# Optimization experiments

Measured on AMD Instinct MI355X. Metric: run time of the kernel, lower is better.

Reference implementation:

```python
import jax, jax.numpy as jnp
import numpy as np

ALPHA = 2.0


def _sq_edt_1d(f):
    """1D squared Euclidean distance transform along the last axis.
    f: (..., n) with 0 at 'sites' and a large value elsewhere.
    g[..., i] = min_j f[..., j] + (i - j)^2  (exact, brute-force lower envelope).
    Uses a scan over output index i to keep memory at O(size(f)).
    """
    n = f.shape[-1]
    idx = jnp.arange(n, dtype=f.dtype)

    def step(_, i):
        return None, jnp.min(f + (i - idx) ** 2, axis=-1)

    _, g = jax.lax.scan(step, None, idx)  # (n, ...)
    return jnp.moveaxis(g, 0, -1)


def _edt(mask):
    """Exact Euclidean distance transform of a boolean mask (b,1,X,Y,Z):
    distance from each True voxel to the nearest False voxel (scipy edt semantics).
    Separable squared-distance transform applied along each spatial axis.
    """
    spatial = mask.shape[2:]
    BIG = jnp.float32(sum(s * s for s in spatial) + 1)  # > any achievable sq dist
    f = jnp.where(mask, BIG, jnp.float32(0.0))
    for ax in range(2, mask.ndim):  # channel axis has size 1 -> contributes 0
        f = jnp.moveaxis(_sq_edt_1d(jnp.moveaxis(f, ax, -1)), -1, ax)
    return jnp.sqrt(f)


def _distance_field(img):
    fg = img > 0.5
    # per-sample guard: field is zero if a sample has no foreground
    fg_any = jnp.any(fg, axis=tuple(range(1, img.ndim)))  # (b,)
    field = _edt(fg) + _edt(~fg)
    shape = (-1,) + (1,) * (img.ndim - 1)
    return jnp.where(fg_any.reshape(shape), field, jnp.float32(0.0))


def setup_inputs() -> dict:
    key = jax.random.key(0)
    k1, k2 = jax.random.split(key)
    pred = jax.random.uniform(k1, (2, 1, 128, 128, 128), dtype=jnp.float32)
    target = jax.random.uniform(k2, (2, 1, 128, 128, 128), dtype=jnp.float32)
    return {"pred": pred, "target": target}


def reference(pred, target):
    # distance fields are computed under no_grad in the original
    pred_dt = jax.lax.stop_gradient(_distance_field(pred))
    target_dt = jax.lax.stop_gradient(_distance_field(target))

    pred_error = (pred - target) ** 2
    distance = pred_dt ** ALPHA + target_dt ** ALPHA
    dt_field = pred_error * distance
    return jnp.mean(dt_field)
```

## Files before the change

### kernel.cpp

```cpp
#include <hip/hip_runtime.h>


constexpr int BIGI = 49153;
constexpr int NVOX = 4194304;
constexpr int STZ  = 129;
constexpr int STX  = 65;

__device__ __forceinline__ void envelope_win(const unsigned int* __restrict__ p,
                                             const int stride, const float i0f,
                                             const int qlo, const int qhi,
                                             float acc[16]) {
    unsigned int vc = p[qlo * stride];
    float jm2 = -4.0f * (float)qlo;
    for (int q = qlo; q <= qhi; ++q) {
        unsigned int vn = p[(q + 1) * stride];
        float h0 = (float)(vc & 0xffffu);
        float h1 = (float)(vc >> 16);
        float jb = jm2 - 2.0f;
        float c0 = fmaf(jm2, i0f, h0);
        float c1 = fmaf(jb,  i0f, h1);
#pragma unroll
        for (int k = 0; k < 16; ++k) {
            acc[k] = fminf(acc[k], fminf(c0, c1));
            c0 += jm2; c1 += jb;
        }
        jm2 -= 4.0f;
        vc = vn;
    }
}

__device__ __forceinline__ int window_of(const unsigned int* __restrict__ p,
                                         const int stride, const int i0) {
    int fmx = 0;
#pragma unroll
    for (int m = 0; m < 8; ++m) {
        unsigned int v = p[((i0 >> 1) + m) * stride];
        int y0 = i0 + 2 * m, y1 = y0 + 1;
        int f0 = (int)(v & 0xffffu) - y0 * y0;
        int f1 = (int)(v >> 16) - y1 * y1;
        fmx = max(fmx, max(f0, f1));
    }
#pragma unroll
    for (int off = 32; off; off >>= 1) fmx = max(fmx, __shfl_xor(fmx, off));
    int W = (int)sqrtf((float)fmx);
    W += (W * W < fmx);
    W += (W * W < fmx);
    return W;
}

__global__ __launch_bounds__(512) void zy_kernel(const float* __restrict__ pred,
                                                 const float* __restrict__ tgt,
                                                 unsigned short* __restrict__ ws) {
    __shared__ unsigned int hz[65 * STZ];
    __shared__ unsigned long long bm[256];
    const int t   = blockIdx.x;
    const int pol = t & 1;
    const int img = (t >> 1) & 1;
    const int s   = t >> 2;
    const int b   = s >> 7;
    const int x   = s & 127;
    const int sb  = (b * 128 + x) * 16384;
    const int tid = threadIdx.x;
    const float* im = img ? tgt : pred;

    float vreg[32];
#pragma unroll
    for (int k = 0; k < 32; ++k) vreg[k] = im[sb + tid + k * 512];

#pragma unroll
    for (int k = 0; k < 32; ++k) {
        bool fg = vreg[k] > 0.5f;
        bool site = pol ? fg : !fg;
        unsigned long long bal = __ballot(site);
        if ((tid & 63) == 0) bm[(tid + k * 512) >> 6] = bal;
    }
    __syncthreads();

    unsigned short* hu = (unsigned short*)hz;
    const int z = tid & 127;
#pragma unroll
    for (int k = 0; k < 32; ++k) {
        int y = (tid >> 7) + k * 4;
        unsigned long long m0 = bm[2 * y], m1 = bm[2 * y + 1];
        int d;
        if (z < 64) {
            unsigned long long lm = m0 << (63 - z);
            unsigned long long rm = m0 >> z;
            int dfwd = lm ? __builtin_clzll(lm) : 999;
            int db0  = rm ? __builtin_ctzll(rm) : 999;
            int db1  = (m1 ? __builtin_ctzll(m1) : 999) + (64 - z);
            d = min(dfwd, min(db0, db1));
        } else {
            int zz = z - 64;
            unsigned long long lm = m1 << (63 - zz);
            unsigned long long rm = m1 >> zz;
            int df1 = lm ? __builtin_clzll(lm) : 999;
            int df0 = (m0 ? __builtin_clzll(m0) : 999) + zz + 1;
            int dbw = rm ? __builtin_ctzll(rm) : 999;
            d = min(min(df1, df0), dbw);
        }
        int f = (d <= 127) ? d * d : BIGI;
        hu[((y >> 1) * STZ) * 2 + (y & 1) + 2 * z] = (unsigned short)(f + y * y);
    }
    __syncthreads();

    unsigned short* outv = ws + (size_t)(img * 2 + pol) * NVOX + sb;
    const int c = tid & 127;
    const int xsq = x * x;
#pragma clang loop unroll(disable)
    for (int r = 0; r < 2; ++r) {
        const int i0 = (tid >> 7) * 16 + r * 64;
        const float i0f = (float)i0;
        const int W = window_of(hz + c, STZ, i0);
        const int qlo = __builtin_amdgcn_readfirstlane(max(0, (i0 - W) >> 1));
        const int qhi = __builtin_amdgcn_readfirstlane(min(63, (i0 + 15 + W) >> 1));
        float acc[16];
#pragma unroll
        for (int k = 0; k < 16; ++k) acc[k] = 3.0e38f;
        envelope_win(hz + c, STZ, i0f, qlo, qhi, acc);
#pragma unroll
        for (int k = 0; k < 16; ++k) {
            float iif = i0f + (float)k;
            outv[(i0 + k) * 128 + c] =
                (unsigned short)((unsigned int)fmaf(iif, iif, acc[k]) + xsq);
        }
    }
}

__global__ __launch_bounds__(512) void xloss_kernel(const float* __restrict__ pred,
                                                    const float* __restrict__ tgt,
                                                    const unsigned short* __restrict__ ws,
                                                    float* __restrict__ out) {
    __shared__ unsigned int hx[129 * STX];
    __shared__ float red[8];
    const int t    = blockIdx.x;
    const int img  = t & 1;
    const int b    = (t >> 1) & 1;
    const int q0   = (t >> 2) * 64;
    const int base = b * 2097152 + q0;
    const int tid  = threadIdx.x;
    const int c    = tid & 63;
    const int i0   = (tid >> 6) * 16;
    const float i0f = (float)i0;
    const unsigned short* A16 = ws + (size_t)(img * 2) * NVOX;
    const unsigned int* A32 = (const unsigned int*)(A16 + base);
    const unsigned int* B32 = (const unsigned int*)(A16 + NVOX + base);

    float dv[16];
#pragma unroll
    for (int k = 0; k < 16; ++k) {
        int v = base + (i0 + k) * 16384 + c;
        dv[k] = pred[v] - tgt[v];
    }

#pragma unroll
    for (int k = 0; k < 8; ++k) {
        int l = tid + k * 512;
        int j = l >> 5, cp = l & 31;
        unsigned int va = A32[j * 8192 + cp];
        unsigned int vb = B32[j * 8192 + cp];
        int w0 = j * STX + 2 * cp;
        hx[w0]     = (va & 0xffffu) | (vb << 16);
        hx[w0 + 1] = (va >> 16)    | (vb & 0xffff0000u);
    }
    __syncthreads();

    const unsigned int* p = hx + c;
    int fmxA = 0, fmxB = 0;
#pragma unroll
    for (int m = 0; m < 16; ++m) {
        int j = i0 + m;
        unsigned int w = p[j * STX];
        fmxA = max(fmxA, (int)(w & 0xffffu) - j * j);
        fmxB = max(fmxB, (int)(w >> 16) - j * j);
    }
    int fmx = max(fmxA, fmxB);
#pragma unroll
    for (int off = 32; off; off >>= 1) {
        fmx  = max(fmx,  __shfl_xor(fmx,  off));
        fmxB = max(fmxB, __shfl_xor(fmxB, off));
    }
    int W = (int)sqrtf((float)fmx);
    W += (W * W < fmx);
    W += (W * W < fmx);
    const int jlo = __builtin_amdgcn_readfirstlane(max(0, i0 - W));
    const int jhi = __builtin_amdgcn_readfirstlane(min(127, i0 + 15 + W));
    const bool nofg = (fmxB >= BIGI);

    float accA[16], accB[16];
#pragma unroll
    for (int k = 0; k < 16; ++k) { accA[k] = 3.0e38f; accB[k] = 3.0e38f; }
    unsigned int vc = p[jlo * STX];
    float jm = -2.0f * (float)jlo;
    for (int j = jlo; j <= jhi; ++j) {
        unsigned int vn = p[(j + 1) * STX];
        float hA = (float)(vc & 0xffffu);
        float hB = (float)(vc >> 16);
        float cA = fmaf(jm, i0f, hA);
        float cB = fmaf(jm, i0f, hB);
#pragma unroll
        for (int k = 0; k < 16; ++k) {
            accA[k] = fminf(accA[k], cA);
            accB[k] = fminf(accB[k], cB);
            cA += jm; cB += jm;
        }
        jm -= 2.0f;
        vc = vn;
    }

    float s = 0.0f;
#pragma unroll
    for (int k = 0; k < 16; ++k) {
        float iif = i0f + (float)k;
        float gA = fmaf(iif, iif, accA[k]);
        float gB = fmaf(iif, iif, accB[k]);
        float d = dv[k];
        float fld = sqrtf(gA) + sqrtf(gB);
        s += d * d * fld * fld;
    }
    if (nofg) s = 0.0f;
#pragma unroll
    for (int off = 32; off > 0; off >>= 1) s += __shfl_down(s, off);
    if ((tid & 63) == 0) red[tid >> 6] = s;
    __syncthreads();
    if (tid == 0) {
        float tot = 0.0f;
#pragma unroll
        for (int w = 0; w < 8; ++w) tot += red[w];
        atomicAdd(out, tot * (1.0f / 4194304.0f));
    }
}

extern "C" void kernel_launch(void* const* d_in, const int* in_sizes, int n_in,
                              void* d_out, int out_size, void* d_ws, size_t ws_size,
                              hipStream_t stream) {
    const float* pred = (const float*)d_in[0];
    const float* tgt  = (const float*)d_in[1];
    float* out = (float*)d_out;
    unsigned short* ws16 = (unsigned short*)d_ws;

    hipMemsetAsync(out, 0, sizeof(float), stream);
    zy_kernel<<<dim3(1024), 512, 0, stream>>>(pred, tgt, ws16);
    xloss_kernel<<<dim3(1024), 512, 0, stream>>>(pred, tgt, ws16, out);
}
```

Measured before the change: 150.8 us.

## Zero output inside first kernel and use per-lane FMA in z-envelope loop

Measured after the change: 154.4 us. 2.4% more time.

```diff
diff --git a/kernel.cpp b/kernel.cpp
--- a/kernel.cpp
+++ b/kernel.cpp
@@ -5,9 +5,11 @@
 constexpr int NVOX = 4194304;
 constexpr int STZ  = 129;
 constexpr int STX  = 65;
-
-__device__ __forceinline__ void envelope_win(const unsigned int* __restrict__ p,
-                                             const int stride, const float i0f,
+constexpr int LDSW = 512 + 65 * STZ;
+
+__device__ __forceinline__ void envelope_fma(const unsigned int* __restrict__ p,
+                                             const int stride,
+                                             const float* __restrict__ ik,
                                              const int qlo, const int qhi,
                                              float acc[16]) {
     unsigned int vc = p[qlo * stride];
@@ -17,12 +19,11 @@
         float h0 = (float)(vc & 0xffffu);
         float h1 = (float)(vc >> 16);
         float jb = jm2 - 2.0f;
-        float c0 = fmaf(jm2, i0f, h0);
-        float c1 = fmaf(jb,  i0f, h1);
 #pragma unroll
         for (int k = 0; k < 16; ++k) {
+            float c0 = fmaf(jm2, ik[k], h0);
+            float c1 = fmaf(jb,  ik[k], h1);
             acc[k] = fminf(acc[k], fminf(c0, c1));
-            c0 += jm2; c1 += jb;
         }
         jm2 -= 4.0f;
         vc = vn;
@@ -50,9 +51,11 @@
 
 __global__ __launch_bounds__(512) void zy_kernel(const float* __restrict__ pred,
                                                  const float* __restrict__ tgt,
-                                                 unsigned short* __restrict__ ws) {
-    __shared__ unsigned int hz[65 * STZ];
-    __shared__ unsigned long long bm[256];
+                                                 unsigned short* __restrict__ ws,
+                                                 float* __restrict__ out) {
+    __shared__ __align__(16) unsigned int lds[LDSW];
+    unsigned long long* bm = (unsigned long long*)lds;
+    unsigned int* hz = lds + 512;
     const int t   = blockIdx.x;
     const int pol = t & 1;
     const int img = (t >> 1) & 1;
@@ -62,6 +65,7 @@
     const int sb  = (b * 128 + x) * 16384;
     const int tid = threadIdx.x;
     const float* im = img ? tgt : pred;
+    if (t == 0 && tid == 0) out[0] = 0.0f;
 
     float vreg[32];
 #pragma unroll
@@ -111,18 +115,20 @@
     for (int r = 0; r < 2; ++r) {
         const int i0 = (tid >> 7) * 16 + r * 64;
         const float i0f = (float)i0;
+        float ik[16];
+#pragma unroll
+        for (int k = 0; k < 16; ++k) ik[k] = i0f + (float)k;
         const int W = window_of(hz + c, STZ, i0);
         const int qlo = __builtin_amdgcn_readfirstlane(max(0, (i0 - W) >> 1));
         const int qhi = __builtin_amdgcn_readfirstlane(min(63, (i0 + 15 + W) >> 1));
         float acc[16];
 #pragma unroll
         for (int k = 0; k < 16; ++k) acc[k] = 3.0e38f;
-        envelope_win(hz + c, STZ, i0f, qlo, qhi, acc);
+        envelope_fma(hz + c, STZ, ik, qlo, qhi, acc);
 #pragma unroll
         for (int k = 0; k < 16; ++k) {
-            float iif = i0f + (float)k;
             outv[(i0 + k) * 128 + c] =
-                (unsigned short)((unsigned int)fmaf(iif, iif, acc[k]) + xsq);
+                (unsigned short)((unsigned int)fmaf(ik[k], ik[k], acc[k]) + xsq);
         }
     }
 }
@@ -131,7 +137,7 @@
                                                     const float* __restrict__ tgt,
                                                     const unsigned short* __restrict__ ws,
                                                     float* __restrict__ out) {
-    __shared__ unsigned int hx[129 * STX];
+    __shared__ __align__(16) unsigned int hx[129 * STX];
     __shared__ float red[8];
     const int t    = blockIdx.x;
     const int img  = t & 1;
@@ -239,7 +245,6 @@
     float* out = (float*)d_out;
     unsigned short* ws16 = (unsigned short*)d_ws;
 
-    hipMemsetAsync(out, 0, sizeof(float), stream);
-    zy_kernel<<<dim3(1024), 512, 0, stream>>>(pred, tgt, ws16);
+    zy_kernel<<<dim3(1024), 512, 0, stream>>>(pred, tgt, ws16, out);
     xloss_kernel<<<dim3(1024), 512, 0, stream>>>(pred, tgt, ws16, out);
 }
```
